# Performance work log

Measured on AMD Instinct MI355X. Metric: run time of the kernel, lower is better.

The kernel has to match this reference:

```python
import jax, jax.numpy as jnp
import numpy as np

N_NODES = 100000
N_EDGES = 1600000
D_IN = 32
D_OUT = 32


def setup_inputs() -> dict:
    key = jax.random.key(0)
    ks = jax.random.split(key, 5)
    feat = jax.random.normal(ks[0], (N_NODES, D_IN), dtype=jnp.float32)
    # xavier_uniform with relu gain, shape (out, in)
    gain = float(np.sqrt(2.0))
    bound = gain * float(np.sqrt(6.0 / (D_IN + D_OUT)))
    W_self = jax.random.uniform(ks[1], (D_OUT, D_IN), minval=-bound, maxval=bound, dtype=jnp.float32)
    W_neigh = jax.random.uniform(ks[2], (D_OUT, D_IN), minval=-bound, maxval=bound, dtype=jnp.float32)
    b_neigh = jnp.zeros((D_OUT,), dtype=jnp.float32)
    src = jax.random.randint(ks[3], (N_EDGES,), 0, N_NODES)
    dst = jax.random.randint(ks[4], (N_EDGES,), 0, N_NODES)
    return {"feat": feat, "W_self": W_self, "W_neigh": W_neigh,
            "b_neigh": b_neigh, "src": src, "dst": dst}


def reference(feat, W_self, W_neigh, b_neigh, src, dst):
    # copy_src + mean aggregation: gather src features, segment-sum into dst,
    # divide by in-degree (0 for isolated dst nodes, matching DGL mean).
    msgs = feat[src]  # [E, D_in] irregular gather
    neigh_sum = jax.ops.segment_sum(msgs, dst, num_segments=N_NODES)  # [N, D_in]
    deg = jax.ops.segment_sum(jnp.ones((dst.shape[0],), feat.dtype), dst,
                              num_segments=N_NODES)  # [N]
    neigh = neigh_sum / jnp.maximum(deg, 1.0)[:, None]
    # GraphSAGE combine: fc_self(h_self) + fc_neigh(neigh)
    rst = feat @ W_self.T + neigh @ W_neigh.T + b_neigh
    return rst
```

## Files before the change

kernel.cpp:

```cpp
#include <hip/hip_runtime.h>

#define D 32
#define BSZ 131
#define PN BSZ
#define BMAX 1024
#define TILE 4096
#define STHREADS 1024
#define CAP 2816
#define TMAX 512
#define APL 17
#define WP 36
#define SF 36
#define DEPTH 12
#define DEPTHH 16

#define FXS2 32768.0f
#define FXINV2 3.0517578125e-05f
#define OFF 8.0f
#define DEGBIAS 262144u

__device__ __forceinline__ unsigned short f2bf(float x) {
    unsigned u = __float_as_uint(x);
    unsigned r = (u + 0x7FFF + ((u >> 16) & 1)) >> 16;
    return (unsigned short)r;
}
__device__ __forceinline__ float bf2f(unsigned short h) {
    return __uint_as_float((unsigned)h << 16);
}
__device__ __forceinline__ unsigned enc(float x) {
    return __float2uint_rn((x + OFF) * FXS2);
}

__global__ __launch_bounds__(STHREADS) void scatter_tiles(
        const int* __restrict__ src, const int* __restrict__ dst,
        int* __restrict__ records, int* __restrict__ startsT,
        const float* __restrict__ feat, unsigned short* __restrict__ featH,
        int E, int Bn, int T, int N, int useH) {
    __shared__ int lhist[STHREADS];
    __shared__ int lofs[BMAX];
    __shared__ int wsum[16];
    __shared__ int stage[TILE];

    int t = threadIdx.x;
    int lane = t & 63;
    int wid = t >> 6;
    int tileStart = blockIdx.x * TILE;

    lhist[t] = 0;
    __syncthreads();

    int sarr[4], darr[4];
    int e0 = tileStart + 4 * t;
    if (tileStart + TILE <= E) {
        int4 s4 = ((const int4*)src)[tileStart / 4 + t];
        int4 d4 = ((const int4*)dst)[tileStart / 4 + t];
        sarr[0] = s4.x; sarr[1] = s4.y; sarr[2] = s4.z; sarr[3] = s4.w;
        darr[0] = d4.x; darr[1] = d4.y; darr[2] = d4.z; darr[3] = d4.w;
    } else {
#pragma unroll
        for (int i = 0; i < 4; ++i) {
            int e = e0 + i;
            sarr[i] = (e < E) ? src[e] : 0;
            darr[i] = (e < E) ? dst[e] : 0;
        }
    }

    int recs[4], bks[4], rr[4];
#pragma unroll
    for (int i = 0; i < 4; ++i) {
        int e = e0 + i;
        if (e < E) {
            int b = (int)((unsigned)darr[i] / (unsigned)BSZ);
            int nl = darr[i] - b * BSZ;
            recs[i] = (sarr[i] << 8) | nl;
            bks[i] = b;
            rr[i] = atomicAdd(&lhist[b], 1);
        } else bks[i] = -1;
    }
    __syncthreads();

    int own = lhist[t];
    int v = own;
#pragma unroll
    for (int off = 1; off < 64; off <<= 1) {
        int u = __shfl_up(v, off, 64);
        if (lane >= off) v += u;
    }
    if (lane == 63) wsum[wid] = v;
    __syncthreads();
    if (wid == 0) {
        int s = (lane < 16) ? wsum[lane] : 0;
#pragma unroll
        for (int off = 1; off < 16; off <<= 1) {
            int u = __shfl_up(s, off, 64);
            if (lane >= off) s += u;
        }
        if (lane < 16) wsum[lane] = s;
    }
    __syncthreads();
    int incl = v + (wid ? wsum[wid - 1] : 0);
    int ex = incl - own;
    if (t <= Bn) startsT[(size_t)t * T + blockIdx.x] = ex;
    if (t < Bn) lofs[t] = ex;
    __syncthreads();

#pragma unroll
    for (int i = 0; i < 4; ++i) {
        if (bks[i] >= 0) stage[lofs[bks[i]] + rr[i]] = recs[i];
    }
    __syncthreads();

    int4* dp = reinterpret_cast<int4*>(records + (size_t)tileStart);
    const int4* sp = reinterpret_cast<const int4*>(stage);
    dp[t] = sp[t];

    if (useH) {
        int total4 = (N * D) >> 2;
        for (int i = blockIdx.x * STHREADS + t; i < total4; i += gridDim.x * STHREADS) {
            float4 f = ((const float4*)feat)[i];
            ushort4 h;
            h.x = f2bf(f.x); h.y = f2bf(f.y); h.z = f2bf(f.z); h.w = f2bf(f.w);
            ((ushort4*)featH)[i] = h;
        }
    }
}

template <bool USEH>
__global__ __launch_bounds__(512) void bucket_final(
        const float* __restrict__ feat, const unsigned short* __restrict__ featH,
        const int* __restrict__ records, const int* __restrict__ startsT,
        const float* __restrict__ Wself, const float* __restrict__ Wneigh,
        const float* __restrict__ bias, float* __restrict__ out,
        int N, int T, int Bn) {
    __shared__ float ubuf[(PN + 1) * SF];
    __shared__ unsigned long long sacc8[((PN + 1) * SF) / 2];
    __shared__ float sWs[D * WP];
    __shared__ float sWn[D * WP];
    __shared__ float sb[D];
    __shared__ int sdeg[PN + 1];
    __shared__ int tstart[TMAX];
    __shared__ int tbase[TMAX + 1];
    __shared__ int wsum2[8];

    int* raw = reinterpret_cast<int*>(ubuf);
    float* sfeatF = ubuf;
    float* saccF = reinterpret_cast<float*>(sacc8);

    int b = blockIdx.x;
    int t = threadIdx.x;
    int lane = t & 63;
    int wid = t >> 6;

    const int NSLOT = PN * 8;
    float4 fr[3];
#pragma unroll
    for (int u = 0; u < 3; ++u) fr[u] = make_float4(0.f, 0.f, 0.f, 0.f);
#pragma unroll
    for (int u = 0; u < 3; ++u) {
        int idx = t + 512 * u;
        if (idx < NSLOT) {
            int n = b * BSZ + (idx >> 3);
            if (n < N) fr[u] = ((const float4*)feat)[(size_t)n * 8 + (idx & 7)];
        }
    }

    for (int i = t; i < ((PN + 1) * SF) / 2; i += 512) sacc8[i] = 0ull;
    if (t <= PN) sdeg[t] = 0;
    for (int i = t; i < D * D; i += 512) {
        int r = i >> 5, c = i & 31;
        sWs[r * WP + c] = Wself[i];
        sWn[r * WP + c] = Wneigh[i];
    }
    if (t < D) sb[t] = bias[t];

    int myc = 0;
    if (t < T) {
        int s0v = startsT[(size_t)b * T + t];
        int s1v = startsT[(size_t)(b + 1) * T + t];
        tstart[t] = s0v;
        myc = s1v - s0v;
    }
    int v = myc;
#pragma unroll
    for (int off = 1; off < 64; off <<= 1) {
        int u = __shfl_up(v, off, 64);
        if (lane >= off) v += u;
    }
    if (lane == 63) wsum2[wid] = v;
    __syncthreads();
    if (wid == 0) {
        int s = (lane < 8) ? wsum2[lane] : 0;
#pragma unroll
        for (int off = 1; off < 8; off <<= 1) {
            int u = __shfl_up(s, off, 64);
            if (lane >= off) s += u;
        }
        if (lane < 8) wsum2[lane] = s;
    }
    __syncthreads();
    int incl = v + (wid ? wsum2[wid - 1] : 0);
    if (t < T) tbase[t] = incl - myc;
    if (t == T - 1) tbase[T] = incl;
    __syncthreads();

    int m = min(tbase[T], CAP);

    int lane4 = t & 3, tg4 = t >> 2;
    for (int tau = tg4; tau < T; tau += 128) {
        int s = tstart[tau];
        int rb = tbase[tau];
        int c2 = tbase[tau + 1] - rb;
        const int* rp = records + (size_t)tau * TILE + s;
        for (int l = lane4; l < c2; l += 4) {
            int pos = rb + l;
            if (pos < CAP) raw[pos] = rp[l];
        }
    }
    __syncthreads();

    int team = t >> 3;
    int part = t & 7;
    if (USEH) {
        for (int base = team; base < m; base += 64 * DEPTHH) {
            ushort4 hv[DEPTHH];
            int nl8[DEPTHH];
            bool ok[DEPTHH];
#pragma unroll
            for (int u = 0; u < DEPTHH; ++u) {
                int idx = base + 64 * u;
                ok[u] = idx < m;
                int rec = raw[ok[u] ? idx : 0];
                int s = rec >> 8;
                nl8[u] = rec & 255;
                hv[u] = *reinterpret_cast<const ushort4*>(
                    featH + (size_t)s * D + part * 4);
            }
#pragma unroll
            for (int u = 0; u < DEPTHH; ++u) {
                if (ok[u]) {
                    unsigned long long* ac = &sacc8[nl8[u] * APL + part * 2];
                    unsigned a0 = enc(bf2f(hv[u].x));
                    unsigned a1 = enc(bf2f(hv[u].y));
                    unsigned a2 = enc(bf2f(hv[u].z));
                    unsigned a3 = enc(bf2f(hv[u].w));
                    atomicAdd(ac + 0, (unsigned long long)a0 | ((unsigned long long)a1 << 32));
                    atomicAdd(ac + 1, (unsigned long long)a2 | ((unsigned long long)a3 << 32));
                    if (part == 0) atomicAdd(&sdeg[nl8[u]], 1);
                }
            }
        }
    } else {
        for (int base = team; base < m; base += 64 * DEPTH) {
            float4 vv[DEPTH];
            int nl8[DEPTH];
            bool ok[DEPTH];
#pragma unroll
            for (int u = 0; u < DEPTH; ++u) {
                int idx = base + 64 * u;
                ok[u] = idx < m;
                int rec = raw[ok[u] ? idx : 0];
                int s = rec >> 8;
                nl8[u] = rec & 255;
                vv[u] = *reinterpret_cast<const float4*>(
                    feat + (size_t)s * D + part * 4);
            }
#pragma unroll
            for (int u = 0; u < DEPTH; ++u) {
                if (ok[u]) {
                    unsigned long long* ac = &sacc8[nl8[u] * APL + part * 2];
                    unsigned a0 = enc(vv[u].x);
                    unsigned a1 = enc(vv[u].y);
                    unsigned a2 = enc(vv[u].z);
                    unsigned a3 = enc(vv[u].w);
                    atomicAdd(ac + 0, (unsigned long long)a0 | ((unsigned long long)a1 << 32));
                    atomicAdd(ac + 1, (unsigned long long)a2 | ((unsigned long long)a3 << 32));
                    if (part == 0) atomicAdd(&sdeg[nl8[u]], 1);
                }
            }
        }
    }
    __syncthreads();

    unsigned rv[9];
    const unsigned* sview = reinterpret_cast<const unsigned*>(sacc8);
#pragma unroll
    for (int r = 0; r < 9; ++r) {
        int i = t + 512 * r;
        if (i < PN * 32) rv[r] = sview[(i >> 5) * (2 * APL) + (i & 31)];
    }
    __syncthreads();
#pragma unroll
    for (int r = 0; r < 9; ++r) {
        int i = t + 512 * r;
        if (i < PN * 32) {
            int node = i >> 5, col = i & 31;
            int iv = (int)(rv[r] - (unsigned)sdeg[node] * DEGBIAS);
            saccF[node * SF + col] = (float)iv * FXINV2;
        }
    }
#pragma unroll
    for (int u = 0; u < 3; ++u) {
        int idx = t + 512 * u;
        if (idx < NSLOT)
            *reinterpret_cast<float4*>(&sfeatF[(idx >> 3) * SF + (idx & 7) * 4]) = fr[u];
    }
    __syncthreads();

    int jp = t & 15;
    int nq = t >> 4;
    int j0 = jp, j1 = jp + 16;
    float b0 = sb[j0], b1 = sb[j1];
    for (int p2 = 0; p2 < 2; ++p2) {
        int q0 = nq + 32 * p2;
        if (q0 * 4 >= PN) break;
        float accS[4][2], accN[4][2];
#pragma unroll
        for (int i = 0; i < 4; ++i) {
            accS[i][0] = 0.f; accS[i][1] = 0.f;
            accN[i][0] = 0.f; accN[i][1] = 0.f;
        }
        const float* fb = &sfeatF[(q0 * 4) * SF];
        const float* nb = &saccF[(q0 * 4) * SF];
#pragma unroll 1
        for (int kk = 0; kk < 8; ++kk) {
            float4 w0 = *reinterpret_cast<const float4*>(&sWs[j0 * WP + kk * 4]);
            float4 w1 = *reinterpret_cast<const float4*>(&sWs[j1 * WP + kk * 4]);
            float4 u0 = *reinterpret_cast<const float4*>(&sWn[j0 * WP + kk * 4]);
            float4 u1 = *reinterpret_cast<const float4*>(&sWn[j1 * WP + kk * 4]);
#pragma unroll
            for (int i = 0; i < 4; ++i) {
                float4 f4 = *reinterpret_cast<const float4*>(&fb[i * SF + kk * 4]);
                float4 n4 = *reinterpret_cast<const float4*>(&nb[i * SF + kk * 4]);
                accS[i][0] += f4.x * w0.x + f4.y * w0.y + f4.z * w0.z + f4.w * w0.w;
                accS[i][1] += f4.x * w1.x + f4.y * w1.y + f4.z * w1.z + f4.w * w1.w;
                accN[i][0] += n4.x * u0.x + n4.y * u0.y + n4.z * u0.z + n4.w * u0.w;
                accN[i][1] += n4.x * u1.x + n4.y * u1.y + n4.z * u1.z + n4.w * u1.w;
            }
        }
#pragma unroll
        for (int i = 0; i < 4; ++i) {
            int nl = q0 * 4 + i;
            int n = b * BSZ + nl;
            if (nl < PN && n < N) {
                float inv = 1.0f / (float)max(sdeg[nl], 1);
                out[(size_t)n * D + j0] = accS[i][0] + inv * accN[i][0] + b0;
                out[(size_t)n * D + j1] = accS[i][1] + inv * accN[i][1] + b1;
            }
        }
    }
}

extern "C" void kernel_launch(void* const* d_in, const int* in_sizes, int n_in,
                              void* d_out, int out_size, void* d_ws, size_t ws_size,
                              hipStream_t stream) {
    const float* feat   = (const float*)d_in[0];
    const float* Wself  = (const float*)d_in[1];
    const float* Wneigh = (const float*)d_in[2];
    const float* bnb    = (const float*)d_in[3];
    const int*   src    = (const int*)d_in[4];
    const int*   dst    = (const int*)d_in[5];

    int N = in_sizes[0] / D;
    int E = in_sizes[4];
    int Bn = (N + BSZ - 1) / BSZ;
    int T  = (E + TILE - 1) / TILE;

    size_t recB = (size_t)T * TILE * sizeof(int);
    size_t stB  = (size_t)(Bn + 1) * T * sizeof(int);
    size_t fhOff = (recB + stB + 63) & ~(size_t)63;
    size_t fhB = (size_t)N * D * sizeof(unsigned short);
    int useH = (fhOff + fhB <= ws_size) ? 1 : 0;

    int* records = (int*)d_ws;
    int* startsT = (int*)((char*)d_ws + recB);
    unsigned short* featH = (unsigned short*)((char*)d_ws + fhOff);

    scatter_tiles<<<T, STHREADS, 0, stream>>>(src, dst, records, startsT,
                                              feat, featH, E, Bn, T, N, useH);
    if (useH)
        bucket_final<true><<<Bn, 512, 0, stream>>>(feat, featH, records, startsT,
                                                   Wself, Wneigh, bnb,
                                                   (float*)d_out, N, T, Bn);
    else
        bucket_final<false><<<Bn, 512, 0, stream>>>(feat, featH, records, startsT,
                                                    Wself, Wneigh, bnb,
                                                    (float*)d_out, N, T, Bn);
}
```

Baseline: 127.2 us.

## Fuse scatter and bucket phases into one cooperative kernel with grid sync

Merges the edge-scatter pass and the per-bucket aggregation/GEMM pass into a single cooperative kernel separated by a grid-wide barrier, with tile count set equal to bucket count (~764 blocks of 512 threads). Tile offsets are stored as 16-bit values to shrink the offset table. The aim is to remove the second launch and its launch gap. The cost is a grid.sync, 512 threads per scatter tile instead of 1024, and a requirement that all blocks be co-resident. If the cooperative launch fails, the code falls back to the old two-kernel path.

Result: slower. 446.3 us (+250.9%).

```diff
diff --git a/kernel.cpp b/kernel.cpp
--- a/kernel.cpp
+++ b/kernel.cpp
@@ -1,13 +1,12 @@
 #include <hip/hip_runtime.h>
+#include <hip/hip_cooperative_groups.h>
+
+namespace cg = cooperative_groups;
 
 #define D 32
 #define BSZ 131
 #define PN BSZ
-#define BMAX 1024
-#define TILE 4096
-#define STHREADS 1024
 #define CAP 2816
-#define TMAX 512
 #define APL 17
 #define WP 36
 #define SF 36
@@ -18,6 +17,11 @@
 #define FXINV2 3.0517578125e-05f
 #define OFF 8.0f
 #define DEGBIAS 262144u
+
+#define TILEF 4096
+#define TMAXF 512
+#define BMAXF 1024
+#define STHREADS 1024
 
 __device__ __forceinline__ unsigned short f2bf(float x) {
     unsigned u = __float_as_uint(x);
@@ -31,27 +35,344 @@
     return __float2uint_rn((x + OFF) * FXS2);
 }
 
-__global__ __launch_bounds__(STHREADS) void scatter_tiles(
+template <bool USEH>
+__global__ __launch_bounds__(512, 6) void sage_fused(
+        const int* __restrict__ src, const int* __restrict__ dst,
+        int* __restrict__ records, unsigned short* __restrict__ startsT,
+        const float* __restrict__ feat, unsigned short* __restrict__ featH,
+        const float* __restrict__ Wself, const float* __restrict__ Wneigh,
+        const float* __restrict__ bias, float* __restrict__ out,
+        int N, int E, int T, int tile2) {
+    __shared__ float ubuf[(PN + 1) * SF];
+    __shared__ unsigned long long sacc8[((PN + 1) * SF) / 2];
+    __shared__ float sWs[D * WP];
+    __shared__ float sWn[D * WP];
+    __shared__ float sb[D];
+    __shared__ int sdeg[PN + 1];
+    __shared__ unsigned short tstart16[768];
+    __shared__ unsigned short tbase16[768];
+    __shared__ int wsum2[8];
+    __shared__ int ctot;
+
+    int t = threadIdx.x;
+    int lane = t & 63;
+    int wid = t >> 6;
+    int bid = blockIdx.x;
+
+    int* stage = reinterpret_cast<int*>(ubuf);
+    int* lhist = reinterpret_cast<int*>(sacc8);
+    int* lofs  = reinterpret_cast<int*>(sacc8) + 768;
+
+    for (int i = t; i <= T; i += 512) lhist[i] = 0;
+    __syncthreads();
+
+    int tileStart = bid * tile2;
+    int cntTile = min(E - tileStart, tile2);
+
+    int recs[5], bks[5], rr[5];
+#pragma unroll
+    for (int i = 0; i < 5; ++i) {
+        int idx = t + i * 512;
+        bks[i] = -1;
+        if (idx < cntTile) {
+            int e = tileStart + idx;
+            int s = src[e], d = dst[e];
+            int b = (int)((unsigned)d / (unsigned)BSZ);
+            int nl = d - b * BSZ;
+            recs[i] = (s << 8) | nl;
+            bks[i] = b;
+            rr[i] = atomicAdd(&lhist[b], 1);
+        }
+    }
+    __syncthreads();
+
+    int mb = 0;
+    for (int chunk = 0; chunk <= T; chunk += 512) {
+        int tt = chunk + t;
+        int own = (tt <= T) ? lhist[tt] : 0;
+        int v = own;
+#pragma unroll
+        for (int off = 1; off < 64; off <<= 1) {
+            int u = __shfl_up(v, off, 64);
+            if (lane >= off) v += u;
+        }
+        if (lane == 63) wsum2[wid] = v;
+        __syncthreads();
+        if (wid == 0) {
+            int s = (lane < 8) ? wsum2[lane] : 0;
+#pragma unroll
+            for (int off = 1; off < 8; off <<= 1) {
+                int u = __shfl_up(s, off, 64);
+                if (lane >= off) s += u;
+            }
+            if (lane < 8) wsum2[lane] = s;
+        }
+        __syncthreads();
+        int incl = v + (wid ? wsum2[wid - 1] : 0);
+        int ex = mb + incl - own;
+        if (tt <= T) {
+            startsT[(size_t)tt * T + bid] = (unsigned short)ex;
+            if (tt < T) lofs[tt] = ex;
+        }
+        if (t == 511) ctot = incl;
+        __syncthreads();
+        mb += ctot;
+    }
+
+#pragma unroll
+    for (int i = 0; i < 5; ++i)
+        if (bks[i] >= 0) stage[lofs[bks[i]] + rr[i]] = recs[i];
+    __syncthreads();
+
+    for (int i = t; i < cntTile; i += 512)
+        records[(size_t)bid * tile2 + i] = stage[i];
+
+    if (USEH) {
+        int total4 = (N * D) >> 2;
+        for (int i = bid * 512 + t; i < total4; i += gridDim.x * 512) {
+            float4 f = ((const float4*)feat)[i];
+            ushort4 h;
+            h.x = f2bf(f.x); h.y = f2bf(f.y); h.z = f2bf(f.z); h.w = f2bf(f.w);
+            ((ushort4*)featH)[i] = h;
+        }
+    }
+
+    __threadfence();
+    cg::this_grid().sync();
+    __threadfence();
+
+    int b = bid;
+    int* raw = reinterpret_cast<int*>(ubuf);
+    float* sfeatF = ubuf;
+    float* saccF = reinterpret_cast<float*>(sacc8);
+
+    const int NSLOT = PN * 8;
+    float4 fr[3];
+#pragma unroll
+    for (int u = 0; u < 3; ++u) fr[u] = make_float4(0.f, 0.f, 0.f, 0.f);
+#pragma unroll
+    for (int u = 0; u < 3; ++u) {
+        int idx = t + 512 * u;
+        if (idx < NSLOT) {
+            int n = b * BSZ + (idx >> 3);
+            if (n < N) fr[u] = ((const float4*)feat)[(size_t)n * 8 + (idx & 7)];
+        }
+    }
+
+    for (int i = t; i < ((PN + 1) * SF) / 2; i += 512) sacc8[i] = 0ull;
+    if (t <= PN) sdeg[t] = 0;
+    for (int i = t; i < D * D; i += 512) {
+        int r = i >> 5, c = i & 31;
+        sWs[r * WP + c] = Wself[i];
+        sWn[r * WP + c] = Wneigh[i];
+    }
+    if (t < D) sb[t] = bias[t];
+
+    int mb2 = 0;
+    for (int chunk = 0; chunk < T; chunk += 512) {
+        int tt = chunk + t;
+        int myc = 0;
+        if (tt < T) {
+            int s0v = startsT[(size_t)b * T + tt];
+            int s1v = startsT[(size_t)(b + 1) * T + tt];
+            tstart16[tt] = (unsigned short)s0v;
+            myc = s1v - s0v;
+        }
+        int v = myc;
+#pragma unroll
+        for (int off = 1; off < 64; off <<= 1) {
+            int u = __shfl_up(v, off, 64);
+            if (lane >= off) v += u;
+        }
+        if (lane == 63) wsum2[wid] = v;
+        __syncthreads();
+        if (wid == 0) {
+            int s = (lane < 8) ? wsum2[lane] : 0;
+#pragma unroll
+            for (int off = 1; off < 8; off <<= 1) {
+                int u = __shfl_up(s, off, 64);
+                if (lane >= off) s += u;
+            }
+            if (lane < 8) wsum2[lane] = s;
+        }
+        __syncthreads();
+        int incl = v + (wid ? wsum2[wid - 1] : 0);
+        if (tt < T) tbase16[tt] = (unsigned short)(mb2 + incl - myc);
+        if (t == 511) ctot = incl;
+        __syncthreads();
+        mb2 += ctot;
+    }
+    if (t == 0) tbase16[T] = (unsigned short)mb2;
+    __syncthreads();
+
+    int m = min(mb2, CAP);
+
+    int lane4 = t & 3, tg4 = t >> 2;
+    for (int tau = tg4; tau < T; tau += 128) {
+        int s = tstart16[tau];
+        int rb = tbase16[tau];
+        int c2 = (int)tbase16[tau + 1] - rb;
+        const int* rp = records + (size_t)tau * tile2 + s;
+        for (int l = lane4; l < c2; l += 4) {
+            int pos = rb + l;
+            if (pos < CAP) raw[pos] = rp[l];
+        }
+    }
+    __syncthreads();
+
+    int team = t >> 3;
+    int part = t & 7;
+    if (USEH) {
+        for (int base = team; base < m; base += 64 * DEPTHH) {
+            ushort4 hv[DEPTHH];
+            int nl8[DEPTHH];
+            bool ok[DEPTHH];
+#pragma unroll
+            for (int u = 0; u < DEPTHH; ++u) {
+                int idx = base + 64 * u;
+                ok[u] = idx < m;
+                int rec = raw[ok[u] ? idx : 0];
+                int s = rec >> 8;
+                nl8[u] = rec & 255;
+                hv[u] = *reinterpret_cast<const ushort4*>(
+                    featH + (size_t)s * D + part * 4);
+            }
+#pragma unroll
+            for (int u = 0; u < DEPTHH; ++u) {
+                if (ok[u]) {
+                    unsigned long long* ac = &sacc8[nl8[u] * APL + part * 2];
+                    unsigned a0 = enc(bf2f(hv[u].x));
+                    unsigned a1 = enc(bf2f(hv[u].y));
+                    unsigned a2 = enc(bf2f(hv[u].z));
+                    unsigned a3 = enc(bf2f(hv[u].w));
+                    atomicAdd(ac + 0, (unsigned long long)a0 | ((unsigned long long)a1 << 32));
+                    atomicAdd(ac + 1, (unsigned long long)a2 | ((unsigned long long)a3 << 32));
+                    if (part == 0) atomicAdd(&sdeg[nl8[u]], 1);
+                }
+            }
+        }
+    } else {
+        for (int base = team; base < m; base += 64 * DEPTH) {
+            float4 vv[DEPTH];
+            int nl8[DEPTH];
+            bool ok[DEPTH];
+#pragma unroll
+            for (int u = 0; u < DEPTH; ++u) {
+                int idx = base + 64 * u;
+                ok[u] = idx < m;
+                int rec = raw[ok[u] ? idx : 0];
+                int s = rec >> 8;
+                nl8[u] = rec & 255;
+                vv[u] = *reinterpret_cast<const float4*>(
+                    feat + (size_t)s * D + part * 4);
+            }
+#pragma unroll
+            for (int u = 0; u < DEPTH; ++u) {
+                if (ok[u]) {
+                    unsigned long long* ac = &sacc8[nl8[u] * APL + part * 2];
+                    unsigned a0 = enc(vv[u].x);
+                    unsigned a1 = enc(vv[u].y);
+                    unsigned a2 = enc(vv[u].z);
+                    unsigned a3 = enc(vv[u].w);
+                    atomicAdd(ac + 0, (unsigned long long)a0 | ((unsigned long long)a1 << 32));
+                    atomicAdd(ac + 1, (unsigned long long)a2 | ((unsigned long long)a3 << 32));
+                    if (part == 0) atomicAdd(&sdeg[nl8[u]], 1);
+                }
+            }
+        }
+    }
+    __syncthreads();
+
+    unsigned rv[9];
+    const unsigned* sview = reinterpret_cast<const unsigned*>(sacc8);
+#pragma unroll
+    for (int r = 0; r < 9; ++r) {
+        int i = t + 512 * r;
+        if (i < PN * 32) rv[r] = sview[(i >> 5) * (2 * APL) + (i & 31)];
+    }
+    __syncthreads();
+#pragma unroll
+    for (int r = 0; r < 9; ++r) {
+        int i = t + 512 * r;
+        if (i < PN * 32) {
+            int node = i >> 5, col = i & 31;
+            int iv = (int)(rv[r] - (unsigned)sdeg[node] * DEGBIAS);
+            saccF[node * SF + col] = (float)iv * FXINV2;
+        }
+    }
+#pragma unroll
+    for (int u = 0; u < 3; ++u) {
+        int idx = t + 512 * u;
+        if (idx < NSLOT)
+            *reinterpret_cast<float4*>(&sfeatF[(idx >> 3) * SF + (idx & 7) * 4]) = fr[u];
+    }
+    __syncthreads();
+
+    int jp = t & 15;
+    int nq = t >> 4;
+    int j0 = jp, j1 = jp + 16;
+    float b0 = sb[j0], b1 = sb[j1];
+    for (int p2 = 0; p2 < 2; ++p2) {
+        int q0 = nq + 32 * p2;
+        if (q0 * 4 >= PN) break;
+        float accS[4][2], accN[4][2];
+#pragma unroll
+        for (int i = 0; i < 4; ++i) {
+            accS[i][0] = 0.f; accS[i][1] = 0.f;
+            accN[i][0] = 0.f; accN[i][1] = 0.f;
+        }
+        const float* fb = &sfeatF[(q0 * 4) * SF];
+        const float* nb = &saccF[(q0 * 4) * SF];
+#pragma unroll 1
+        for (int kk = 0; kk < 8; ++kk) {
+            float4 w0 = *reinterpret_cast<const float4*>(&sWs[j0 * WP + kk * 4]);
+            float4 w1 = *reinterpret_cast<const float4*>(&sWs[j1 * WP + kk * 4]);
+            float4 u0 = *reinterpret_cast<const float4*>(&sWn[j0 * WP + kk * 4]);
+            float4 u1 = *reinterpret_cast<const float4*>(&sWn[j1 * WP + kk * 4]);
+#pragma unroll
+            for (int i = 0; i < 4; ++i) {
+                float4 f4 = *reinterpret_cast<const float4*>(&fb[i * SF + kk * 4]);
+                float4 n4 = *reinterpret_cast<const float4*>(&nb[i * SF + kk * 4]);
+                accS[i][0] += f4.x * w0.x + f4.y * w0.y + f4.z * w0.z + f4.w * w0.w;
+                accS[i][1] += f4.x * w1.x + f4.y * w1.y + f4.z * w1.z + f4.w * w1.w;
+                accN[i][0] += n4.x * u0.x + n4.y * u0.y + n4.z * u0.z + n4.w * u0.w;
+                accN[i][1] += n4.x * u1.x + n4.y * u1.y + n4.z * u1.z + n4.w * u1.w;
+            }
+        }
+#pragma unroll
+        for (int i = 0; i < 4; ++i) {
+            int nl = q0 * 4 + i;
+            int n = b * BSZ + nl;
+            if (nl < PN && n < N) {
+                float inv = 1.0f / (float)max(sdeg[nl], 1);
+                out[(size_t)n * D + j0] = accS[i][0] + inv * accN[i][0] + b0;
+                out[(size_t)n * D + j1] = accS[i][1] + inv * accN[i][1] + b1;
+            }
+        }
+    }
+}
+
+__global__ __launch_bounds__(STHREADS) void scatter_tiles_fb(
         const int* __restrict__ src, const int* __restrict__ dst,
         int* __restrict__ records, int* __restrict__ startsT,
         const float* __restrict__ feat, unsigned short* __restrict__ featH,
         int E, int Bn, int T, int N, int useH) {
     __shared__ int lhist[STHREADS];
-    __shared__ int lofs[BMAX];
+    __shared__ int lofs[BMAXF];
     __shared__ int wsum[16];
-    __shared__ int stage[TILE];
+    __shared__ int stage[TILEF];
 
     int t = threadIdx.x;
     int lane = t & 63;
     int wid = t >> 6;
-    int tileStart = blockIdx.x * TILE;
+    int tileStart = blockIdx.x * TILEF;
 
     lhist[t] = 0;
     __syncthreads();
 
     int sarr[4], darr[4];
     int e0 = tileStart + 4 * t;
-    if (tileStart + TILE <= E) {
+    if (tileStart + TILEF <= E) {
         int4 s4 = ((const int4*)src)[tileStart / 4 + t];
         int4 d4 = ((const int4*)dst)[tileStart / 4 + t];
         sarr[0] = s4.x; sarr[1] = s4.y; sarr[2] = s4.z; sarr[3] = s4.w;
@@ -126,7 +447,7 @@
 }
 
 template <bool USEH>
-__global__ __launch_bounds__(512) void bucket_final(
+__global__ __launch_bounds__(512) void bucket_final_fb(
         const float* __restrict__ feat, const unsigned short* __restrict__ featH,
         const int* __restrict__ records, const int* __restrict__ startsT,
         const float* __restrict__ Wself, const float* __restrict__ Wneigh,
@@ -138,8 +459,8 @@
     __shared__ float sWn[D * WP];
     __shared__ float sb[D];
     __shared__ int sdeg[PN + 1];
-    __shared__ int tstart[TMAX];
-    __shared__ int tbase[TMAX + 1];
+    __shared__ int tstart[TMAXF];
+    __shared__ int tbase[TMAXF + 1];
     __shared__ int wsum2[8];
 
     int* raw = reinterpret_cast<int*>(ubuf);
@@ -210,7 +531,7 @@
         int s = tstart[tau];
         int rb = tbase[tau];
         int c2 = tbase[tau + 1] - rb;
-        const int* rp = records + (size_t)tau * TILE + s;
+        const int* rp = records + (size_t)tau * TILEF + s;
         for (int l = lane4; l < c2; l += 4) {
             int pos = rb + l;
             if (pos < CAP) raw[pos] = rp[l];
@@ -359,30 +680,57 @@
     const float* bnb    = (const float*)d_in[3];
     const int*   src    = (const int*)d_in[4];
     const int*   dst    = (const int*)d_in[5];
+    float* outp = (float*)d_out;
 
     int N = in_sizes[0] / D;
     int E = in_sizes[4];
     int Bn = (N + BSZ - 1) / BSZ;
-    int T  = (E + TILE - 1) / TILE;
-
-    size_t recB = (size_t)T * TILE * sizeof(int);
-    size_t stB  = (size_t)(Bn + 1) * T * sizeof(int);
-    size_t fhOff = (recB + stB + 63) & ~(size_t)63;
+
+    int Tc = Bn;
+    int tile2 = (E + Tc - 1) / Tc;
+    size_t recBc = (size_t)Tc * tile2 * sizeof(int);
+    size_t stBc  = (size_t)(Tc + 1) * Tc * sizeof(unsigned short);
+    size_t fhOffc = (recBc + stBc + 63) & ~(size_t)63;
     size_t fhB = (size_t)N * D * sizeof(unsigned short);
-    int useH = (fhOff + fhB <= ws_size) ? 1 : 0;
-
-    int* records = (int*)d_ws;
-    int* startsT = (int*)((char*)d_ws + recB);
-    unsigned short* featH = (unsigned short*)((char*)d_ws + fhOff);
-
-    scatter_tiles<<<T, STHREADS, 0, stream>>>(src, dst, records, startsT,
-                                              feat, featH, E, Bn, T, N, useH);
-    if (useH)
-        bucket_final<true><<<Bn, 512, 0, stream>>>(feat, featH, records, startsT,
-                                                   Wself, Wneigh, bnb,
-                                                   (float*)d_out, N, T, Bn);
+    int useHc = (fhOffc + fhB <= ws_size) ? 1 : 0;
+
+    int* recordsC = (int*)d_ws;
+    unsigned short* startsTC = (unsigned short*)((char*)d_ws + recBc);
+    unsigned short* featHC = (unsigned short*)((char*)d_ws + fhOffc);
+
+    void* args[] = {(void*)&src, (void*)&dst, (void*)&recordsC, (void*)&startsTC,
+                    (void*)&feat, (void*)&featHC, (void*)&Wself, (void*)&Wneigh,
+                    (void*)&bnb, (void*)&outp, (void*)&N, (void*)&E, (void*)&Tc,
+                    (void*)&tile2};
+
+    hipError_t err;
+    if (useHc)
+        err = hipLaunchCooperativeKernel(
+            reinterpret_cast<const void*>(&sage_fused<true>),
+            dim3(Tc), dim3(512), args, 0, stream);
     else
-        bucket_final<false><<<Bn, 512, 0, stream>>>(feat, featH, records, startsT,
-                                                    Wself, Wneigh, bnb,
-                                                    (float*)d_out, N, T, Bn);
+        err = hipLaunchCooperativeKernel(
+            reinterpret_cast<const void*>(&sage_fused<false>),
+            dim3(Tc), dim3(512), args, 0, stream);
+
+    if (err != hipSuccess) {
+        int T = (E + TILEF - 1) / TILEF;
+        size_t recB = (size_t)T * TILEF * sizeof(int);
+        size_t stB  = (size_t)(Bn + 1) * T * sizeof(int);
+        size_t fhOff = (recB + stB + 63) & ~(size_t)63;
+        int useH = (fhOff + fhB <= ws_size) ? 1 : 0;
+
+        int* records = (int*)d_ws;
+        int* startsT = (int*)((char*)d_ws + recB);
+        unsigned short* featH = (unsigned short*)((char*)d_ws + fhOff);
+
+        scatter_tiles_fb<<<T, STHREADS, 0, stream>>>(src, dst, records, startsT,
+                                                     feat, featH, E, Bn, T, N, useH);
+        if (useH)
+            bucket_final_fb<true><<<Bn, 512, 0, stream>>>(feat, featH, records, startsT,
+                                                          Wself, Wneigh, bnb, outp, N, T, Bn);
+        else
+            bucket_final_fb<false><<<Bn, 512, 0, stream>>>(feat, featH, records, startsT,
+                                                           Wself, Wneigh, bnb, outp, N, T, Bn);
+    }
 }
```
